# Performance work log

Hardware: AMD Instinct MI355X
Metric: run time of the kernel (lower is better)

The kernel has to match this reference:

```python
import jax, jax.numpy as jnp
import numpy as np

N_NODES = 100000


def setup_inputs() -> dict:
    key = jax.random.key(0)
    k1, k2, k3 = jax.random.split(key, 3)
    x = jax.random.normal(k1, (N_NODES, 256), dtype=jnp.float32)
    edge_index = jax.random.randint(k2, (2, 1600000), 0, N_NODES, dtype=jnp.int64)
    W = jax.random.normal(k3, (256, 128), dtype=jnp.float32) * (1.0 / np.sqrt(256.0))
    b = jnp.zeros((128,), dtype=jnp.float32)
    alpha = jnp.full((128,), 0.25, dtype=jnp.float32)  # PReLU default init
    return {"x": x, "edge_index": edge_index, "W": W, "b": b, "alpha": alpha}


def reference(x, edge_index, W, b, alpha):
    N = x.shape[0]
    # --- GCNConv: add self-loops ---
    loops = jnp.arange(N, dtype=edge_index.dtype)
    row = jnp.concatenate([edge_index[0], loops])  # source nodes
    col = jnp.concatenate([edge_index[1], loops])  # destination nodes
    # symmetric normalization: deg computed at destinations (self-loops => deg >= 1)
    deg = jax.ops.segment_sum(jnp.ones(col.shape, x.dtype), col, num_segments=N)
    dinv = jax.lax.rsqrt(deg)
    norm = dinv[row] * dinv[col]  # [E+N]
    # linear transform then normalized scatter-add aggregation
    h = x @ W  # [N, H]
    msg = h[row] * norm[:, None]  # [E+N, H]
    out = jax.ops.segment_sum(msg, col, num_segments=N) + b  # bias after aggregation
    # --- PReLU (per-channel) ---
    return jnp.where(out >= 0, out, alpha * out)
```

## Files before the change

### kernel.cpp

```cpp
#include <hip/hip_runtime.h>

constexpr int KDIM  = 256;
constexpr int HDIM  = 128;
constexpr int BK    = 128;
constexpr int CHUNK = 8192;
constexpr int NBMAX = 800;

typedef __bf16 bf16x8 __attribute__((ext_vector_type(8)));
typedef float  f32x4  __attribute__((ext_vector_type(4)));

__device__ __forceinline__ ushort f2bf(float f) {
    unsigned u = __float_as_uint(f);
    unsigned r = (u + 0x7fffu + ((u >> 16) & 1u)) >> 16;
    return (ushort)r;
}

__device__ __forceinline__ void accum8(float* a, uint4 u) {
    a[0] += __uint_as_float(u.x << 16); a[1] += __uint_as_float(u.x & 0xffff0000u);
    a[2] += __uint_as_float(u.y << 16); a[3] += __uint_as_float(u.y & 0xffff0000u);
    a[4] += __uint_as_float(u.z << 16); a[5] += __uint_as_float(u.z & 0xffff0000u);
    a[6] += __uint_as_float(u.w << 16); a[7] += __uint_as_float(u.w & 0xffff0000u);
}

__global__ __launch_bounds__(512) void prep_sort_kernel(
    const float* __restrict__ W, ushort* __restrict__ Wt, ushort* __restrict__ hsb,
    const int* __restrict__ row, const int* __restrict__ col,
    uint* __restrict__ ebuf, int* __restrict__ histG, int* __restrict__ localOff,
    int n, int e, int nbv, int gblk) {
    __shared__ uint dst[CHUNK];
    __shared__ int hist[NBMAX], excl[NBMAX], cur[NBMAX];
    __shared__ int ws2[8];
    int b = blockIdx.x, t = threadIdx.x;
    if (b < 8) {
        int g = b * 512 + t;
        int lane = g & 63, cn = g >> 6;
        int c = cn >> 3, nf = cn & 7;
        int ncol = nf * 16 + (lane & 15);
        int k0 = c * 32 + (lane >> 4) * 8;
        ushort* dp = Wt + (size_t)g * 8;
        #pragma unroll
        for (int j = 0; j < 8; ++j) dp[j] = f2bf(W[(k0 + j) * HDIM + ncol]);
        return;
    }
    if (b == 8) {
        if (t < HDIM) hsb[(size_t)n * HDIM + t] = 0;
        return;
    }
    int g = b - 9;
    int lane = t & 63, w = t >> 6;
    for (int i = t; i < nbv; i += 512) hist[i] = 0;
    __syncthreads();
    int lo = g * CHUNK, hi = min(lo + CHUNK, e);
    int colr[16];
    #pragma unroll
    for (int k = 0; k < 4; ++k) {
        int i0 = lo + (k * 512 + t) * 4;
        if (i0 + 3 < hi) {
            int4 c4 = *(const int4*)(col + i0);
            colr[k * 4 + 0] = c4.x; colr[k * 4 + 1] = c4.y;
            colr[k * 4 + 2] = c4.z; colr[k * 4 + 3] = c4.w;
            atomicAdd(&hist[c4.x >> 7], 1); atomicAdd(&hist[c4.y >> 7], 1);
            atomicAdd(&hist[c4.z >> 7], 1); atomicAdd(&hist[c4.w >> 7], 1);
        } else {
            #pragma unroll
            for (int j = 0; j < 4; ++j) {
                int i = i0 + j;
                int c = (i < hi) ? col[i] : -1;
                colr[k * 4 + j] = c;
                if (c >= 0) atomicAdd(&hist[c >> 7], 1);
            }
        }
    }
    __syncthreads();
    {
        int b0 = t * 2;
        int h0 = (b0 < nbv) ? hist[b0] : 0;
        int h1 = (b0 + 1 < nbv) ? hist[b0 + 1] : 0;
        int s = h0 + h1, incl = s;
        #pragma unroll
        for (int d = 1; d < 64; d <<= 1) { int u = __shfl_up(incl, d, 64); if (lane >= d) incl += u; }
        if (lane == 63) ws2[w] = incl;
        __syncthreads();
        int add = 0;
        #pragma unroll
        for (int i = 0; i < 8; ++i) if (i < w) add += ws2[i];
        int run = add + incl - s;
        if (b0 < nbv)     { excl[b0] = run;          cur[b0] = run; }
        if (b0 + 1 < nbv) { excl[b0 + 1] = run + h0; cur[b0 + 1] = run + h0; }
    }
    __syncthreads();
    #pragma unroll
    for (int k = 0; k < 4; ++k) {
        int i0 = lo + (k * 512 + t) * 4;
        if (i0 + 3 < hi) {
            int4 r4 = *(const int4*)(row + i0);
            int rr[4] = {r4.x, r4.y, r4.z, r4.w};
            #pragma unroll
            for (int j = 0; j < 4; ++j) {
                int c = colr[k * 4 + j];
                int p = atomicAdd(&cur[c >> 7], 1);
                dst[p] = ((uint)rr[j] << 7) | (uint)(c & 127);
            }
        } else {
            #pragma unroll
            for (int j = 0; j < 4; ++j) {
                int i = i0 + j, c = colr[k * 4 + j];
                if (c >= 0) {
                    int p = atomicAdd(&cur[c >> 7], 1);
                    dst[p] = ((uint)row[i] << 7) | (uint)(c & 127);
                }
            }
        }
    }
    __syncthreads();
    int cnt = hi - lo;
    for (int k = 0; k < 4; ++k) {
        int i0 = (k * 512 + t) * 4;
        if (i0 + 3 < cnt) *(uint4*)(ebuf + lo + i0) = *(uint4*)&dst[i0];
        else for (int j = 0; j < 4; ++j) if (i0 + j < cnt) ebuf[lo + i0 + j] = dst[i0 + j];
    }
    for (int i = t; i < nbv; i += 512) {
        histG[i * gblk + g]    = hist[i];
        localOff[i * gblk + g] = excl[i];
    }
}

__global__ __launch_bounds__(256) void scanA_kernel(const int* __restrict__ in,
                                                    int* __restrict__ partial, int n) {
    int t = threadIdx.x, base = blockIdx.x * 1024;
    int s = 0;
    #pragma unroll
    for (int j = 0; j < 4; ++j) {
        int i = base + j * 256 + t;
        if (i < n) s += in[i];
    }
    __shared__ int ws[4];
    #pragma unroll
    for (int d = 1; d < 64; d <<= 1) s += __shfl_xor(s, d, 64);
    int lane = t & 63, w = t >> 6;
    if (lane == 0) ws[w] = s;
    __syncthreads();
    if (t == 0) partial[blockIdx.x] = ws[0] + ws[1] + ws[2] + ws[3];
}

__global__ void scanB_kernel(int* __restrict__ partial, int nb) {
    int t = threadIdx.x;
    int v = (t < nb) ? partial[t] : 0;
    int orig = v;
    int lane = t & 63, w = t >> 6;
    #pragma unroll
    for (int d = 1; d < 64; d <<= 1) { int u = __shfl_up(v, d, 64); if (lane >= d) v += u; }
    __shared__ int ws[4];
    if (lane == 63) ws[w] = v;
    __syncthreads();
    int add = 0;
    #pragma unroll
    for (int i = 0; i < 4; ++i) if (i < w) add += ws[i];
    if (t < nb) partial[t] = v + add - orig;
}

__global__ __launch_bounds__(256) void scanC_kernel(const int* __restrict__ in,
                                                    const int* __restrict__ partial,
                                                    int* __restrict__ out, int n) {
    int t = threadIdx.x, base = blockIdx.x * 1024;
    int vals[4], tsum = 0;
    #pragma unroll
    for (int j = 0; j < 4; ++j) {
        int i = base + t * 4 + j;
        vals[j] = (i < n) ? in[i] : 0;
        tsum += vals[j];
    }
    int lane = t & 63, w = t >> 6;
    int incl = tsum;
    #pragma unroll
    for (int d = 1; d < 64; d <<= 1) { int u = __shfl_up(incl, d, 64); if (lane >= d) incl += u; }
    __shared__ int ws[4];
    if (lane == 63) ws[w] = incl;
    __syncthreads();
    int add = partial[blockIdx.x];
    #pragma unroll
    for (int i = 0; i < 4; ++i) if (i < w) add += ws[i];
    int run = add + incl - tsum;
    #pragma unroll
    for (int j = 0; j < 4; ++j) {
        int i = base + t * 4 + j;
        if (i < n) out[i] = run;
        run += vals[j];
    }
}

__global__ __launch_bounds__(256) void fine_kernel(const uint* __restrict__ ebuf,
                                                   const int* __restrict__ histG,
                                                   const int* __restrict__ localOff,
                                                   const int* __restrict__ histS,
                                                   uint* __restrict__ csr,
                                                   int* __restrict__ deg,
                                                   int* __restrict__ offs,
                                                   float* __restrict__ dinv,
                                                   int e, int nbv, int gblk, int n) {
    __shared__ uint elist[4096];
    __shared__ uint csrl[4096];
    __shared__ int hist[BK], excl[BK], cur[BK];
    int b = blockIdx.x, t = threadIdx.x;
    int seg0 = histS[b * gblk];
    int seg1 = (b + 1 < nbv) ? histS[(b + 1) * gblk] : e;
    int cnt = min(seg1 - seg0, 4096);

    if (t < BK) { hist[t] = 0; cur[t] = 0; }
    for (int g = t; g < gblk; g += 256) {
        int c   = histG[b * gblk + g];
        int src = g * CHUNK + localOff[b * gblk + g];
        int dst = histS[b * gblk + g] - seg0;
        for (int i = 0; i < c; ++i) elist[dst + i] = ebuf[src + i];
    }
    __syncthreads();
    for (int i = t; i < cnt; i += 256) atomicAdd(&hist[elist[i] & 127], 1);
    __syncthreads();
    if (t < 64) {
        int v0 = hist[2 * t], v1 = hist[2 * t + 1];
        int s = v0 + v1, incl = s;
        #pragma unroll
        for (int d = 1; d < 64; d <<= 1) { int u = __shfl_up(incl, d, 64); if (t >= d) incl += u; }
        int base = incl - s;
        excl[2 * t] = base; excl[2 * t + 1] = base + v0;
    }
    __syncthreads();
    for (int i = t; i < cnt; i += 256) {
        uint v = elist[i];
        int d = v & 127;
        int r = atomicAdd(&cur[d], 1);
        csrl[excl[d] + r] = v >> 7;
    }
    __syncthreads();
    for (int i = t; i < cnt; i += 256) csr[seg0 + i] = csrl[i];
    if (t < BK) {
        int node = b * BK + t;
        if (node < n) {
            int dg = hist[t];
            deg[node]  = dg;
            offs[node] = seg0 + excl[t];
            dinv[node] = rsqrtf((float)(dg + 1));
        }
    }
}


constexpr int MT = 64;
constexpr int XS_STRIDE = 264;

__global__ __launch_bounds__(256) void gemm_kernel(const float* __restrict__ x,
                                                   const ushort* __restrict__ Wt,
                                                   const float* __restrict__ dinv,
                                                   ushort* __restrict__ hsb, int n) {
    __shared__ ushort xs[MT * XS_STRIDE];
    __shared__ float sdinv[MT];
    int t = threadIdx.x, lane = t & 63, w = t >> 6;
    int row0 = blockIdx.x * MT;

    bf16x8 bfrag[8][2];
    #pragma unroll
    for (int c = 0; c < 8; ++c)
        #pragma unroll
        for (int f = 0; f < 2; ++f)
            bfrag[c][f] = *(const bf16x8*)(Wt + (size_t)(((c * 8) + (w * 2 + f)) * 64 + lane) * 8);

    #pragma unroll
    for (int i = 0; i < 16; ++i) {
        int rl = w * 16 + i;
        int gr = row0 + rl; if (gr >= n) gr = n - 1;
        float4 v = *(const float4*)(x + (size_t)gr * KDIM + lane * 4);
        ushort4 o;
        o.x = f2bf(v.x); o.y = f2bf(v.y); o.z = f2bf(v.z); o.w = f2bf(v.w);
        *(ushort4*)(xs + rl * XS_STRIDE + lane * 4) = o;
    }
    if (t < MT) { int g = row0 + t; sdinv[t] = dinv[(g < n) ? g : (n - 1)]; }
    __syncthreads();

    #pragma unroll
    for (int s = 0; s < MT / 16; ++s) {
        f32x4 acc0 = {0.f, 0.f, 0.f, 0.f}, acc1 = {0.f, 0.f, 0.f, 0.f};
        #pragma unroll
        for (int c = 0; c < 8; ++c) {
            const ushort* ap = xs + (s * 16 + (lane & 15)) * XS_STRIDE + c * 32 + (lane >> 4) * 8;
            bf16x8 afrag = *(const bf16x8*)ap;
            acc0 = __builtin_amdgcn_mfma_f32_16x16x32_bf16(afrag, bfrag[c][0], acc0, 0, 0, 0);
            acc1 = __builtin_amdgcn_mfma_f32_16x16x32_bf16(afrag, bfrag[c][1], acc1, 0, 0, 0);
        }
        #pragma unroll
        for (int reg = 0; reg < 4; ++reg) {
            int rl = s * 16 + (lane >> 4) * 4 + reg;
            int gr = row0 + rl;
            if (gr < n) {
                float d = sdinv[rl];
                int col0 = w * 32 + (lane & 15);
                hsb[(size_t)gr * HDIM + col0]      = f2bf(acc0[reg] * d);
                hsb[(size_t)gr * HDIM + col0 + 16] = f2bf(acc1[reg] * d);
            }
        }
    }
}


__global__ __launch_bounds__(256) void aggregate_kernel(
    const ushort* __restrict__ hsb, const int* __restrict__ offs,
    const int* __restrict__ deg, const int* __restrict__ csr,
    const float* __restrict__ dinv, const float* __restrict__ b,
    const float* __restrict__ alpha, float* __restrict__ out, int n) {
    int wv = threadIdx.x >> 6, lane = threadIdx.x & 63;
    int grp = lane >> 4, li = lane & 15;
    int node = blockIdx.x * 16 + wv * 4 + grp;
    bool valid = node < n;
    int nd   = valid ? node : n;
    int base = valid ? offs[node] : 0;
    int cnt  = valid ? deg[node] : 0;
    const uint4* hs4 = (const uint4*)hsb;

    float a[8];
    #pragma unroll
    for (int i = 0; i < 8; ++i) a[i] = 0.f;

    uint4 su = hs4[(size_t)nd * 16 + li];
    accum8(a, su);

    for (int it = 0; it < cnt; it += 4) {
        int src_l = (li < 4 && (it + li) < cnt) ? (int)csr[base + it + li] : n;
        int s0 = __shfl(src_l, grp * 16 + 0, 64);
        int s1 = __shfl(src_l, grp * 16 + 1, 64);
        int s2 = __shfl(src_l, grp * 16 + 2, 64);
        int s3 = __shfl(src_l, grp * 16 + 3, 64);
        uint4 u0 = hs4[(size_t)s0 * 16 + li];
        uint4 u1 = hs4[(size_t)s1 * 16 + li];
        uint4 u2 = hs4[(size_t)s2 * 16 + li];
        uint4 u3 = hs4[(size_t)s3 * 16 + li];
        accum8(a, u0); accum8(a, u1); accum8(a, u2); accum8(a, u3);
    }

    if (valid) {
        float dc = dinv[node];
        int c0 = li * 8;
        float o[8];
        #pragma unroll
        for (int i = 0; i < 8; ++i) {
            float v = fmaf(dc, a[i], b[c0 + i]);
            o[i] = v >= 0.f ? v : alpha[c0 + i] * v;
        }
        float* op = out + (size_t)node * HDIM + c0;
        *(float4*)op       = make_float4(o[0], o[1], o[2], o[3]);
        *(float4*)(op + 4) = make_float4(o[4], o[5], o[6], o[7]);
    }
}


extern "C" void kernel_launch(void* const* d_in, const int* in_sizes, int n_in,
                              void* d_out, int out_size, void* d_ws, size_t ws_size,
                              hipStream_t stream) {
    const float* x     = (const float*)d_in[0];
    const int*   ei    = (const int*)d_in[1];
    const float* W     = (const float*)d_in[2];
    const float* b     = (const float*)d_in[3];
    const float* alpha = (const float*)d_in[4];
    float* out = (float*)d_out;

    int E = in_sizes[1] / 2;
    int N = in_sizes[0] / KDIM;
    int NB = (N + BK - 1) / BK;
    int GBLK = (E + CHUNK - 1) / CHUNK;
    int SCAN_N = NB * GBLK;

    ushort* hsb   = (ushort*)d_ws;
    ushort* Wt    = hsb + (size_t)(N + 1) * HDIM;
    float* dinv   = (float*)(Wt + 32768);
    int* deg      = (int*)(dinv + N);
    int* offs     = deg + N;
    int* histG    = offs + N;
    int* localOff = histG + SCAN_N;
    int* histS    = localOff + SCAN_N;
    int* partial  = histS + SCAN_N;
    uint* ebuf    = (uint*)(partial + 512);
    uint* csr     = ebuf + (size_t)GBLK * CHUNK;

    const int* rowp = ei;
    const int* colp = ei + E;

    int nbScan = (SCAN_N + 1023) / 1024;

    hipLaunchKernelGGL(prep_sort_kernel, dim3(9 + GBLK), dim3(512), 0, stream,
                       W, Wt, hsb, rowp, colp, ebuf, histG, localOff, N, E, NB, GBLK);
    hipLaunchKernelGGL(scanA_kernel, dim3(nbScan), dim3(256), 0, stream, histG, partial, SCAN_N);
    hipLaunchKernelGGL(scanB_kernel, dim3(1), dim3(256), 0, stream, partial, nbScan);
    hipLaunchKernelGGL(scanC_kernel, dim3(nbScan), dim3(256), 0, stream, histG, partial, histS, SCAN_N);
    hipLaunchKernelGGL(fine_kernel, dim3(NB), dim3(256), 0, stream,
                       ebuf, histG, localOff, histS, csr, deg, offs, dinv, E, NB, GBLK, N);
    hipLaunchKernelGGL(gemm_kernel, dim3((N + MT - 1) / MT), dim3(256), 0, stream, x, Wt, dinv, hsb, N);
    hipLaunchKernelGGL(aggregate_kernel, dim3((N + 15) / 16), dim3(256), 0, stream,
                       hsb, offs, deg, (const int*)csr, dinv, b, alpha, out, N);
}
```

Before: 295.9 us.

## Split hidden features into eight column planes and aggregate per plane slice

The bf16 transformed features move from row-major layout into eight planes of 16 columns each. The GEMM writes into these planes. The aggregation kernel now gives each block one plane slice, with two lanes per node covering 16 columns. Each slice's working set is about 3.2 MB, which is meant to fit in cache and turn the random neighbor gathers into cache hits. Neighbor indices are now loaded directly per lane with a one-step prefetch instead of shuffles, and non-temporal hints are added. In exchange, the CSR index list is read eight times, and each gather fetches only 32 bytes.

```diff
diff --git a/kernel.cpp b/kernel.cpp
--- a/kernel.cpp
+++ b/kernel.cpp
@@ -21,6 +21,7 @@
     a[4] += __uint_as_float(u.z << 16); a[5] += __uint_as_float(u.z & 0xffff0000u);
     a[6] += __uint_as_float(u.w << 16); a[7] += __uint_as_float(u.w & 0xffff0000u);
 }
+
 
 __global__ __launch_bounds__(512) void prep_sort_kernel(
     const float* __restrict__ W, ushort* __restrict__ Wt, ushort* __restrict__ hsb,
@@ -43,7 +44,10 @@
         return;
     }
     if (b == 8) {
-        if (t < HDIM) hsb[(size_t)n * HDIM + t] = 0;
+        if (t < HDIM) {
+            size_t PS = (size_t)(n + 1) * 16;
+            hsb[(size_t)(t >> 4) * PS + (size_t)n * 16 + (t & 15)] = 0;
+        }
         return;
     }
     int g = b - 9;
@@ -276,6 +280,7 @@
     if (t < MT) { int g = row0 + t; sdinv[t] = dinv[(g < n) ? g : (n - 1)]; }
     __syncthreads();
 
+    size_t PS = (size_t)(n + 1) * 16;
     #pragma unroll
     for (int s = 0; s < MT / 16; ++s) {
         f32x4 acc0 = {0.f, 0.f, 0.f, 0.f}, acc1 = {0.f, 0.f, 0.f, 0.f};
@@ -292,52 +297,65 @@
             int gr = row0 + rl;
             if (gr < n) {
                 float d = sdinv[rl];
-                int col0 = w * 32 + (lane & 15);
-                hsb[(size_t)gr * HDIM + col0]      = f2bf(acc0[reg] * d);
-                hsb[(size_t)gr * HDIM + col0 + 16] = f2bf(acc1[reg] * d);
+                int r = lane & 15;
+                hsb[(size_t)(2 * w) * PS + (size_t)gr * 16 + r]     = f2bf(acc0[reg] * d);
+                hsb[(size_t)(2 * w + 1) * PS + (size_t)gr * 16 + r] = f2bf(acc1[reg] * d);
             }
         }
     }
 }
 
+
+#define LDC4(itv, dst)                                                                   \
+    do {                                                                                 \
+        int _i = (itv);                                                                  \
+        dst.x = (_i     < cnt) ? __builtin_nontemporal_load(csr + base + _i)     : zn;   \
+        dst.y = (_i + 1 < cnt) ? __builtin_nontemporal_load(csr + base + _i + 1) : zn;   \
+        dst.z = (_i + 2 < cnt) ? __builtin_nontemporal_load(csr + base + _i + 2) : zn;   \
+        dst.w = (_i + 3 < cnt) ? __builtin_nontemporal_load(csr + base + _i + 3) : zn;   \
+    } while (0)
 
 __global__ __launch_bounds__(256) void aggregate_kernel(
     const ushort* __restrict__ hsb, const int* __restrict__ offs,
-    const int* __restrict__ deg, const int* __restrict__ csr,
+    const int* __restrict__ deg, const uint* __restrict__ csr,
     const float* __restrict__ dinv, const float* __restrict__ b,
     const float* __restrict__ alpha, float* __restrict__ out, int n) {
-    int wv = threadIdx.x >> 6, lane = threadIdx.x & 63;
-    int grp = lane >> 4, li = lane & 15;
-    int node = blockIdx.x * 16 + wv * 4 + grp;
+    int slice = blockIdx.x & 7;
+    int nb    = blockIdx.x >> 3;
+    int w = threadIdx.x >> 6, lane = threadIdx.x & 63;
+    int slot = lane >> 1, li = lane & 1;
+    int node = nb * 128 + w * 32 + slot;
     bool valid = node < n;
-    int nd   = valid ? node : n;
-    int base = valid ? offs[node] : 0;
-    int cnt  = valid ? deg[node] : 0;
-    const uint4* hs4 = (const uint4*)hsb;
+    int base = valid ? __builtin_nontemporal_load(offs + node) : 0;
+    int cnt  = valid ? __builtin_nontemporal_load(deg + node) : 0;
+    uint zn = (uint)n;
+
+    size_t PS4 = (size_t)(n + 1) * 2;
+    const uint4* pl = (const uint4*)hsb + (size_t)slice * PS4;
 
     float a[8];
     #pragma unroll
     for (int i = 0; i < 8; ++i) a[i] = 0.f;
 
-    uint4 su = hs4[(size_t)nd * 16 + li];
+    uint4 su = pl[(size_t)(valid ? node : n) * 2 + li];
     accum8(a, su);
 
+    uint4 c4;
+    c4.x = c4.y = c4.z = c4.w = zn;
+    if (cnt > 0) LDC4(0, c4);
     for (int it = 0; it < cnt; it += 4) {
-        int src_l = (li < 4 && (it + li) < cnt) ? (int)csr[base + it + li] : n;
-        int s0 = __shfl(src_l, grp * 16 + 0, 64);
-        int s1 = __shfl(src_l, grp * 16 + 1, 64);
-        int s2 = __shfl(src_l, grp * 16 + 2, 64);
-        int s3 = __shfl(src_l, grp * 16 + 3, 64);
-        uint4 u0 = hs4[(size_t)s0 * 16 + li];
-        uint4 u1 = hs4[(size_t)s1 * 16 + li];
-        uint4 u2 = hs4[(size_t)s2 * 16 + li];
-        uint4 u3 = hs4[(size_t)s3 * 16 + li];
+        uint4 cur = c4;
+        if (it + 4 < cnt) LDC4(it + 4, c4);
+        uint4 u0 = pl[(size_t)cur.x * 2 + li];
+        uint4 u1 = pl[(size_t)cur.y * 2 + li];
+        uint4 u2 = pl[(size_t)cur.z * 2 + li];
+        uint4 u3 = pl[(size_t)cur.w * 2 + li];
         accum8(a, u0); accum8(a, u1); accum8(a, u2); accum8(a, u3);
     }
 
     if (valid) {
-        float dc = dinv[node];
-        int c0 = li * 8;
+        float dc = __builtin_nontemporal_load(dinv + node);
+        int c0 = slice * 16 + li * 8;
         float o[8];
         #pragma unroll
         for (int i = 0; i < 8; ++i) {
@@ -345,8 +363,10 @@
             o[i] = v >= 0.f ? v : alpha[c0 + i] * v;
         }
         float* op = out + (size_t)node * HDIM + c0;
-        *(float4*)op       = make_float4(o[0], o[1], o[2], o[3]);
-        *(float4*)(op + 4) = make_float4(o[4], o[5], o[6], o[7]);
+        f32x4 v0 = {o[0], o[1], o[2], o[3]};
+        f32x4 v1 = {o[4], o[5], o[6], o[7]};
+        __builtin_nontemporal_store(v0, (f32x4*)op);
+        __builtin_nontemporal_store(v1, (f32x4*)(op + 4));
     }
 }
 
@@ -383,6 +403,7 @@
     const int* colp = ei + E;
 
     int nbScan = (SCAN_N + 1023) / 1024;
+    int nbAgg  = (N + 127) / 128;
 
     hipLaunchKernelGGL(prep_sort_kernel, dim3(9 + GBLK), dim3(512), 0, stream,
                        W, Wt, hsb, rowp, colp, ebuf, histG, localOff, N, E, NB, GBLK);
@@ -392,6 +413,6 @@
     hipLaunchKernelGGL(fine_kernel, dim3(NB), dim3(256), 0, stream,
                        ebuf, histG, localOff, histS, csr, deg, offs, dinv, E, NB, GBLK, N);
     hipLaunchKernelGGL(gemm_kernel, dim3((N + MT - 1) / MT), dim3(256), 0, stream, x, Wt, dinv, hsb, N);
-    hipLaunchKernelGGL(aggregate_kernel, dim3((N + 15) / 16), dim3(256), 0, stream,
-                       hsb, offs, deg, (const int*)csr, dinv, b, alpha, out, N);
-}
+    hipLaunchKernelGGL(aggregate_kernel, dim3(8 * nbAgg), dim3(256), 0, stream,
+                       hsb, offs, deg, csr, dinv, b, alpha, out, N);
+}
```

Result: slower. 397.1 us (+34.2%).

## Restructure edge bucketing with global bucket counters and fuse fine sort into aggregation

Applied to the files above, without the earlier changes.

Replaces the per-chunk histogram plus three-kernel scan with a global bucket count pass, a single-block scan, and a scatter kernel that reserves space in each bucket through global atomic cursors. The per-bucket fine sort moves into the aggregation kernel, so CSR is built in shared memory and consumed directly instead of being written to and reread from global memory. A small kernel recomputes degrees for dinv before the GEMM. Aggregation now handles 128 nodes per block with 8 gathers in flight and nontemporal stores. In exchange, edges are read twice for histogramming and the bucketing adds global atomic contention.

```diff
diff --git a/kernel.cpp b/kernel.cpp
--- a/kernel.cpp
+++ b/kernel.cpp
@@ -22,14 +22,10 @@
     a[6] += __uint_as_float(u.w << 16); a[7] += __uint_as_float(u.w & 0xffff0000u);
 }
 
-__global__ __launch_bounds__(512) void prep_sort_kernel(
+__global__ __launch_bounds__(512) void prep_kernel(
     const float* __restrict__ W, ushort* __restrict__ Wt, ushort* __restrict__ hsb,
-    const int* __restrict__ row, const int* __restrict__ col,
-    uint* __restrict__ ebuf, int* __restrict__ histG, int* __restrict__ localOff,
-    int n, int e, int nbv, int gblk) {
-    __shared__ uint dst[CHUNK];
-    __shared__ int hist[NBMAX], excl[NBMAX], cur[NBMAX];
-    __shared__ int ws2[8];
+    const int* __restrict__ col, int* __restrict__ bucketCnt, int n, int e, int nbv) {
+    __shared__ int hist[NBMAX];
     int b = blockIdx.x, t = threadIdx.x;
     if (b < 8) {
         int g = b * 512 + t;
@@ -47,6 +43,58 @@
         return;
     }
     int g = b - 9;
+    for (int i = t; i < nbv; i += 512) hist[i] = 0;
+    __syncthreads();
+    int lo = g * CHUNK, hi = min(lo + CHUNK, e);
+    #pragma unroll
+    for (int k = 0; k < 4; ++k) {
+        int i0 = lo + (k * 512 + t) * 4;
+        if (i0 + 3 < hi) {
+            int4 c4 = *(const int4*)(col + i0);
+            atomicAdd(&hist[c4.x >> 7], 1); atomicAdd(&hist[c4.y >> 7], 1);
+            atomicAdd(&hist[c4.z >> 7], 1); atomicAdd(&hist[c4.w >> 7], 1);
+        } else {
+            for (int j = 0; j < 4; ++j) {
+                int i = i0 + j;
+                if (i < hi) atomicAdd(&hist[col[i] >> 7], 1);
+            }
+        }
+    }
+    __syncthreads();
+    for (int i = t; i < nbv; i += 512) {
+        int h = hist[i];
+        if (h) atomicAdd(&bucketCnt[i], h);
+    }
+}
+
+__global__ __launch_bounds__(1024) void bscan_kernel(const int* __restrict__ bucketCnt,
+                                                     int* __restrict__ bucketOff,
+                                                     int* __restrict__ gcur, int nbv, int e) {
+    __shared__ int ws[16];
+    int t = threadIdx.x, lane = t & 63, w = t >> 6;
+    int v = (t < nbv) ? bucketCnt[t] : 0;
+    int orig = v;
+    #pragma unroll
+    for (int d = 1; d < 64; d <<= 1) { int u = __shfl_up(v, d, 64); if (lane >= d) v += u; }
+    if (lane == 63) ws[w] = v;
+    __syncthreads();
+    int add = 0;
+    #pragma unroll
+    for (int i = 0; i < 16; ++i) if (i < w) add += ws[i];
+    int excl = v + add - orig;
+    if (t < nbv) { bucketOff[t] = excl; gcur[t] = excl; }
+    if (t == 0)  bucketOff[nbv] = e;
+}
+
+__global__ __launch_bounds__(512) void scatter_kernel(const int* __restrict__ row,
+                                                      const int* __restrict__ col,
+                                                      int* __restrict__ gcur,
+                                                      uint* __restrict__ ebuf,
+                                                      int e, int nbv) {
+    __shared__ uint dst[CHUNK];
+    __shared__ int hist[NBMAX], excl[NBMAX], cur[NBMAX];
+    __shared__ int ws2[8];
+    int g = blockIdx.x, t = threadIdx.x;
     int lane = t & 63, w = t >> 6;
     for (int i = t; i < nbv; i += 512) hist[i] = 0;
     __syncthreads();
@@ -113,134 +161,32 @@
         }
     }
     __syncthreads();
-    int cnt = hi - lo;
-    for (int k = 0; k < 4; ++k) {
-        int i0 = (k * 512 + t) * 4;
-        if (i0 + 3 < cnt) *(uint4*)(ebuf + lo + i0) = *(uint4*)&dst[i0];
-        else for (int j = 0; j < 4; ++j) if (i0 + j < cnt) ebuf[lo + i0 + j] = dst[i0 + j];
-    }
-    for (int i = t; i < nbv; i += 512) {
-        histG[i * gblk + g]    = hist[i];
-        localOff[i * gblk + g] = excl[i];
-    }
-}
-
-__global__ __launch_bounds__(256) void scanA_kernel(const int* __restrict__ in,
-                                                    int* __restrict__ partial, int n) {
-    int t = threadIdx.x, base = blockIdx.x * 1024;
-    int s = 0;
-    #pragma unroll
-    for (int j = 0; j < 4; ++j) {
-        int i = base + j * 256 + t;
-        if (i < n) s += in[i];
-    }
-    __shared__ int ws[4];
-    #pragma unroll
-    for (int d = 1; d < 64; d <<= 1) s += __shfl_xor(s, d, 64);
-    int lane = t & 63, w = t >> 6;
-    if (lane == 0) ws[w] = s;
-    __syncthreads();
-    if (t == 0) partial[blockIdx.x] = ws[0] + ws[1] + ws[2] + ws[3];
-}
-
-__global__ void scanB_kernel(int* __restrict__ partial, int nb) {
-    int t = threadIdx.x;
-    int v = (t < nb) ? partial[t] : 0;
-    int orig = v;
-    int lane = t & 63, w = t >> 6;
-    #pragma unroll
-    for (int d = 1; d < 64; d <<= 1) { int u = __shfl_up(v, d, 64); if (lane >= d) v += u; }
-    __shared__ int ws[4];
-    if (lane == 63) ws[w] = v;
-    __syncthreads();
-    int add = 0;
-    #pragma unroll
-    for (int i = 0; i < 4; ++i) if (i < w) add += ws[i];
-    if (t < nb) partial[t] = v + add - orig;
-}
-
-__global__ __launch_bounds__(256) void scanC_kernel(const int* __restrict__ in,
-                                                    const int* __restrict__ partial,
-                                                    int* __restrict__ out, int n) {
-    int t = threadIdx.x, base = blockIdx.x * 1024;
-    int vals[4], tsum = 0;
-    #pragma unroll
-    for (int j = 0; j < 4; ++j) {
-        int i = base + t * 4 + j;
-        vals[j] = (i < n) ? in[i] : 0;
-        tsum += vals[j];
-    }
-    int lane = t & 63, w = t >> 6;
-    int incl = tsum;
-    #pragma unroll
-    for (int d = 1; d < 64; d <<= 1) { int u = __shfl_up(incl, d, 64); if (lane >= d) incl += u; }
-    __shared__ int ws[4];
-    if (lane == 63) ws[w] = incl;
-    __syncthreads();
-    int add = partial[blockIdx.x];
-    #pragma unroll
-    for (int i = 0; i < 4; ++i) if (i < w) add += ws[i];
-    int run = add + incl - tsum;
-    #pragma unroll
-    for (int j = 0; j < 4; ++j) {
-        int i = base + t * 4 + j;
-        if (i < n) out[i] = run;
-        run += vals[j];
-    }
-}
-
-__global__ __launch_bounds__(256) void fine_kernel(const uint* __restrict__ ebuf,
-                                                   const int* __restrict__ histG,
-                                                   const int* __restrict__ localOff,
-                                                   const int* __restrict__ histS,
-                                                   uint* __restrict__ csr,
-                                                   int* __restrict__ deg,
-                                                   int* __restrict__ offs,
-                                                   float* __restrict__ dinv,
-                                                   int e, int nbv, int gblk, int n) {
-    __shared__ uint elist[4096];
-    __shared__ uint csrl[4096];
-    __shared__ int hist[BK], excl[BK], cur[BK];
+    int grp = t >> 4, li = t & 15;
+    for (int b0 = grp; b0 < nbv; b0 += 32) {
+        int c = hist[b0];
+        if (c == 0) continue;
+        int p;
+        if (li == 0) p = atomicAdd(&gcur[b0], c);
+        p = __shfl(p, lane & ~15, 64);
+        int s = excl[b0];
+        for (int i = li; i < c; i += 16) ebuf[p + i] = dst[s + i];
+    }
+}
+
+__global__ __launch_bounds__(256) void deg_kernel(const uint* __restrict__ ebuf,
+                                                  const int* __restrict__ bucketOff,
+                                                  float* __restrict__ dinv, int n) {
+    __shared__ int hist[BK];
     int b = blockIdx.x, t = threadIdx.x;
-    int seg0 = histS[b * gblk];
-    int seg1 = (b + 1 < nbv) ? histS[(b + 1) * gblk] : e;
-    int cnt = min(seg1 - seg0, 4096);
-
-    if (t < BK) { hist[t] = 0; cur[t] = 0; }
-    for (int g = t; g < gblk; g += 256) {
-        int c   = histG[b * gblk + g];
-        int src = g * CHUNK + localOff[b * gblk + g];
-        int dst = histS[b * gblk + g] - seg0;
-        for (int i = 0; i < c; ++i) elist[dst + i] = ebuf[src + i];
-    }
-    __syncthreads();
-    for (int i = t; i < cnt; i += 256) atomicAdd(&hist[elist[i] & 127], 1);
-    __syncthreads();
-    if (t < 64) {
-        int v0 = hist[2 * t], v1 = hist[2 * t + 1];
-        int s = v0 + v1, incl = s;
-        #pragma unroll
-        for (int d = 1; d < 64; d <<= 1) { int u = __shfl_up(incl, d, 64); if (t >= d) incl += u; }
-        int base = incl - s;
-        excl[2 * t] = base; excl[2 * t + 1] = base + v0;
-    }
-    __syncthreads();
-    for (int i = t; i < cnt; i += 256) {
-        uint v = elist[i];
-        int d = v & 127;
-        int r = atomicAdd(&cur[d], 1);
-        csrl[excl[d] + r] = v >> 7;
-    }
-    __syncthreads();
-    for (int i = t; i < cnt; i += 256) csr[seg0 + i] = csrl[i];
+    int s0 = bucketOff[b], s1 = bucketOff[b + 1];
+    int cnt = min(s1 - s0, 4096);
+    if (t < BK) hist[t] = 0;
+    __syncthreads();
+    for (int i = t; i < cnt; i += 256) atomicAdd(&hist[ebuf[s0 + i] & 127], 1);
+    __syncthreads();
     if (t < BK) {
         int node = b * BK + t;
-        if (node < n) {
-            int dg = hist[t];
-            deg[node]  = dg;
-            offs[node] = seg0 + excl[t];
-            dinv[node] = rsqrtf((float)(dg + 1));
-        }
+        if (node < n) dinv[node] = rsqrtf((float)(hist[t] + 1));
     }
 }
 
@@ -300,53 +246,84 @@
     }
 }
 
-
-__global__ __launch_bounds__(256) void aggregate_kernel(
-    const ushort* __restrict__ hsb, const int* __restrict__ offs,
-    const int* __restrict__ deg, const int* __restrict__ csr,
-    const float* __restrict__ dinv, const float* __restrict__ b,
-    const float* __restrict__ alpha, float* __restrict__ out, int n) {
-    int wv = threadIdx.x >> 6, lane = threadIdx.x & 63;
-    int grp = lane >> 4, li = lane & 15;
-    int node = blockIdx.x * 16 + wv * 4 + grp;
-    bool valid = node < n;
-    int nd   = valid ? node : n;
-    int base = valid ? offs[node] : 0;
-    int cnt  = valid ? deg[node] : 0;
+__global__ __launch_bounds__(256) void agg_kernel(
+    const ushort* __restrict__ hsb, const uint* __restrict__ ebuf,
+    const int* __restrict__ bucketOff, const float* __restrict__ dinv,
+    const float* __restrict__ bias, const float* __restrict__ alpha,
+    float* __restrict__ out, int n) {
+    __shared__ uint elist[4096];
+    __shared__ uint csrl[4096];
+    __shared__ int hist[BK], excl[BK], cur[BK];
+    int b = blockIdx.x, t = threadIdx.x;
+    int s0 = bucketOff[b], s1 = bucketOff[b + 1];
+    int cnt = min(s1 - s0, 4096);
+
+    if (t < BK) { hist[t] = 0; cur[t] = 0; }
+    __syncthreads();
+    for (int i = t; i < cnt; i += 256) {
+        uint v = __builtin_nontemporal_load(ebuf + s0 + i);
+        elist[i] = v;
+        atomicAdd(&hist[v & 127], 1);
+    }
+    __syncthreads();
+    if (t < 64) {
+        int v0 = hist[2 * t], v1 = hist[2 * t + 1];
+        int s = v0 + v1, incl = s;
+        #pragma unroll
+        for (int d = 1; d < 64; d <<= 1) { int u = __shfl_up(incl, d, 64); if (t >= d) incl += u; }
+        int base = incl - s;
+        excl[2 * t] = base; excl[2 * t + 1] = base + v0;
+    }
+    __syncthreads();
+    for (int i = t; i < cnt; i += 256) {
+        uint v = elist[i];
+        int d = v & 127;
+        int r = atomicAdd(&cur[d], 1);
+        csrl[excl[d] + r] = v >> 7;
+    }
+    __syncthreads();
+
+    int grp = t >> 4, li = t & 15;
     const uint4* hs4 = (const uint4*)hsb;
-
-    float a[8];
-    #pragma unroll
-    for (int i = 0; i < 8; ++i) a[i] = 0.f;
-
-    uint4 su = hs4[(size_t)nd * 16 + li];
-    accum8(a, su);
-
-    for (int it = 0; it < cnt; it += 4) {
-        int src_l = (li < 4 && (it + li) < cnt) ? (int)csr[base + it + li] : n;
-        int s0 = __shfl(src_l, grp * 16 + 0, 64);
-        int s1 = __shfl(src_l, grp * 16 + 1, 64);
-        int s2 = __shfl(src_l, grp * 16 + 2, 64);
-        int s3 = __shfl(src_l, grp * 16 + 3, 64);
-        uint4 u0 = hs4[(size_t)s0 * 16 + li];
-        uint4 u1 = hs4[(size_t)s1 * 16 + li];
-        uint4 u2 = hs4[(size_t)s2 * 16 + li];
-        uint4 u3 = hs4[(size_t)s3 * 16 + li];
-        accum8(a, u0); accum8(a, u1); accum8(a, u2); accum8(a, u3);
-    }
-
-    if (valid) {
-        float dc = dinv[node];
-        int c0 = li * 8;
-        float o[8];
-        #pragma unroll
-        for (int i = 0; i < 8; ++i) {
-            float v = fmaf(dc, a[i], b[c0 + i]);
-            o[i] = v >= 0.f ? v : alpha[c0 + i] * v;
-        }
-        float* op = out + (size_t)node * HDIM + c0;
-        *(float4*)op       = make_float4(o[0], o[1], o[2], o[3]);
-        *(float4*)(op + 4) = make_float4(o[4], o[5], o[6], o[7]);
+    for (int nl = grp; nl < BK; nl += 16) {
+        int node = b * BK + nl;
+        bool valid = node < n;
+        int base = excl[nl];
+        int c = hist[nl];
+        float a[8];
+        #pragma unroll
+        for (int i = 0; i < 8; ++i) a[i] = 0.f;
+
+        uint4 su = hs4[(size_t)(valid ? node : n) * 16 + li];
+        accum8(a, su);
+
+        for (int it = 0; it < c; it += 8) {
+            int s[8];
+            #pragma unroll
+            for (int k = 0; k < 8; ++k)
+                s[k] = (it + k < c) ? (int)csrl[base + it + k] : n;
+            uint4 u[8];
+            #pragma unroll
+            for (int k = 0; k < 8; ++k) u[k] = hs4[(size_t)s[k] * 16 + li];
+            #pragma unroll
+            for (int k = 0; k < 8; ++k) accum8(a, u[k]);
+        }
+
+        if (valid) {
+            float dc = dinv[node];
+            int c0 = li * 8;
+            float o[8];
+            #pragma unroll
+            for (int i = 0; i < 8; ++i) {
+                float v = fmaf(dc, a[i], bias[c0 + i]);
+                o[i] = v >= 0.f ? v : alpha[c0 + i] * v;
+            }
+            float* op = out + (size_t)node * HDIM + c0;
+            f32x4 v0 = {o[0], o[1], o[2], o[3]};
+            f32x4 v1 = {o[4], o[5], o[6], o[7]};
+            __builtin_nontemporal_store(v0, (f32x4*)op);
+            __builtin_nontemporal_store(v1, (f32x4*)(op + 4));
+        }
     }
 }
 
@@ -365,33 +342,29 @@
     int N = in_sizes[0] / KDIM;
     int NB = (N + BK - 1) / BK;
     int GBLK = (E + CHUNK - 1) / CHUNK;
-    int SCAN_N = NB * GBLK;
-
-    ushort* hsb   = (ushort*)d_ws;
-    ushort* Wt    = hsb + (size_t)(N + 1) * HDIM;
-    float* dinv   = (float*)(Wt + 32768);
-    int* deg      = (int*)(dinv + N);
-    int* offs     = deg + N;
-    int* histG    = offs + N;
-    int* localOff = histG + SCAN_N;
-    int* histS    = localOff + SCAN_N;
-    int* partial  = histS + SCAN_N;
-    uint* ebuf    = (uint*)(partial + 512);
-    uint* csr     = ebuf + (size_t)GBLK * CHUNK;
+
+    ushort* hsb     = (ushort*)d_ws;
+    ushort* Wt      = hsb + (size_t)(N + 1) * HDIM;
+    float* dinv     = (float*)(Wt + 32768);
+    int* bucketCnt  = (int*)(dinv + N);
+    int* bucketOff  = bucketCnt + NB;
+    int* gcur       = bucketOff + NB + 1;
+    uint* ebuf      = (uint*)(gcur + NB);
 
     const int* rowp = ei;
     const int* colp = ei + E;
 
-    int nbScan = (SCAN_N + 1023) / 1024;
-
-    hipLaunchKernelGGL(prep_sort_kernel, dim3(9 + GBLK), dim3(512), 0, stream,
-                       W, Wt, hsb, rowp, colp, ebuf, histG, localOff, N, E, NB, GBLK);
-    hipLaunchKernelGGL(scanA_kernel, dim3(nbScan), dim3(256), 0, stream, histG, partial, SCAN_N);
-    hipLaunchKernelGGL(scanB_kernel, dim3(1), dim3(256), 0, stream, partial, nbScan);
-    hipLaunchKernelGGL(scanC_kernel, dim3(nbScan), dim3(256), 0, stream, histG, partial, histS, SCAN_N);
-    hipLaunchKernelGGL(fine_kernel, dim3(NB), dim3(256), 0, stream,
-                       ebuf, histG, localOff, histS, csr, deg, offs, dinv, E, NB, GBLK, N);
-    hipLaunchKernelGGL(gemm_kernel, dim3((N + MT - 1) / MT), dim3(256), 0, stream, x, Wt, dinv, hsb, N);
-    hipLaunchKernelGGL(aggregate_kernel, dim3((N + 15) / 16), dim3(256), 0, stream,
-                       hsb, offs, deg, (const int*)csr, dinv, b, alpha, out, N);
-}
+    hipMemsetAsync(bucketCnt, 0, (size_t)NB * sizeof(int), stream);
+    hipLaunchKernelGGL(prep_kernel, dim3(9 + GBLK), dim3(512), 0, stream,
+                       W, Wt, hsb, colp, bucketCnt, N, E, NB);
+    hipLaunchKernelGGL(bscan_kernel, dim3(1), dim3(1024), 0, stream,
+                       bucketCnt, bucketOff, gcur, NB, E);
+    hipLaunchKernelGGL(scatter_kernel, dim3(GBLK), dim3(512), 0, stream,
+                       rowp, colp, gcur, ebuf, E, NB);
+    hipLaunchKernelGGL(deg_kernel, dim3(NB), dim3(256), 0, stream,
+                       ebuf, bucketOff, dinv, N);
+    hipLaunchKernelGGL(gemm_kernel, dim3((N + MT - 1) / MT), dim3(256), 0, stream,
+                       x, Wt, dinv, hsb, N);
+    hipLaunchKernelGGL(agg_kernel, dim3(NB), dim3(256), 0, stream,
+                       hsb, ebuf, bucketOff, dinv, b, alpha, out, N);
+}
```

Result: slower. 347.4 us (+17.4%).
